# Kernel optimization log

Hardware: AMD Instinct MI355X
Metric: run time of the kernel (lower is better)

Reference implementation:

```python
import jax, jax.numpy as jnp
import numpy as np

G, K = 5, 3  # pyKAN defaults: grid intervals, spline order

def b_splines(x, grid, k=K):
    # x: [B, in], grid: [in, G+2k+1] extended knots -> basis [B, in, G+k]
    x = x[..., None]
    B = ((x >= grid[:, :-1]) & (x < grid[:, 1:])).astype(x.dtype)
    for p in range(1, k + 1):  # De Boor / Cox recursion
        B = (x - grid[:, :-(p + 1)]) / (grid[:, p:-1] - grid[:, :-(p + 1)]) * B[..., :-1] \
          + (grid[:, p + 1:] - x) / (grid[:, p + 1:] - grid[:, 1:-p]) * B[..., 1:]
    return B

def kan_layer(x, grid, coef, scale_base, scale_sp):
    # y_j = sum_i scale_base[i,j]*silu(x_i) + scale_sp[i,j]*sum_k coef[i,j,k]*B_k(x_i)
    basis = b_splines(x, grid)                                  # [B, in, G+K]
    y_sp = jnp.einsum('bik,iok,io->bo', basis, coef, scale_sp)
    y_base = jnp.einsum('bi,io->bo', jax.nn.silu(x), scale_base)
    return y_base + y_sp

def _uniform_grid(dim, g=G, k=K):
    h = 2.0 / g
    knots = np.linspace(-1.0 - k * h, 1.0 + k * h, g + 2 * k + 1).astype(np.float32)
    return jnp.tile(jnp.asarray(knots)[None, :], (dim, 1))

def setup_inputs() -> dict:
    key = jax.random.key(0)
    ks = jax.random.split(key, 7)
    B, IN, HID, OUT = 2048, 128, 512, 128
    nb = G + K
    return {
        'state': jax.random.normal(ks[0], (B, IN), jnp.float32),
        'grid1': _uniform_grid(IN),
        'coef1': 0.1 * jax.random.normal(ks[1], (IN, HID, nb), jnp.float32),
        'scale_base1': jax.random.normal(ks[2], (IN, HID), jnp.float32) / np.sqrt(IN).astype(np.float32),
        'scale_sp1': jnp.ones((IN, HID), jnp.float32),
        'grid2': _uniform_grid(HID),
        'coef2': 0.1 * jax.random.normal(ks[3], (HID, OUT, nb), jnp.float32),
        'scale_base2': jax.random.normal(ks[4], (HID, OUT), jnp.float32) / np.sqrt(HID).astype(np.float32),
        'scale_sp2': jnp.ones((HID, OUT), jnp.float32),
    }

def reference(state, grid1, coef1, scale_base1, scale_sp1, grid2, coef2, scale_base2, scale_sp2):
    h = kan_layer(state, grid1, coef1, scale_base1, scale_sp1)
    y = kan_layer(h, grid2, coef2, scale_base2, scale_sp2)
    return y
```

## Files before the change

kernel.cpp:

```cpp
#include <hip/hip_runtime.h>
#include <math.h>

#define BATCH 2048
#define IN1   128
#define HID   512
#define OUT2  128
#define NB    8
#define NKNOT 12
#define K1 (IN1*9)
#define K2 (HID*9)
#define SPLIT2 16
#define KS2 288
#define LDSW 40
#define A2S 296

typedef short s16x8 __attribute__((ext_vector_type(8)));
typedef float f32x4 __attribute__((ext_vector_type(4)));

__device__ inline unsigned short f2bf(float f) {
    unsigned int u = __float_as_uint(f);
    return (unsigned short)((u + 0x7fffu + ((u >> 16) & 1u)) >> 16);
}

__device__ inline void basis8(float x, float* out8) {
    float d[NKNOT];
#pragma unroll
    for (int t = 0; t < NKNOT; ++t) d[t] = x - (0.4f * (float)t - 2.2f);
    float B[NKNOT - 1];
#pragma unroll
    for (int t = 0; t < NKNOT - 1; ++t)
        B[t] = (d[t] >= 0.0f && d[t + 1] < 0.0f) ? 1.0f : 0.0f;
#pragma unroll
    for (int p = 1; p <= 3; ++p) {
        const float c = 1.0f / (0.4f * (float)p);
#pragma unroll
        for (int t = 0; t < NKNOT - 1; ++t)
            if (t < NKNOT - 1 - p)
                B[t] = c * (d[t] * B[t] - d[t + p + 1] * B[t + 1]);
    }
#pragma unroll
    for (int t = 0; t < NB; ++t) out8[t] = B[t];
}

__device__ inline float silu_f(float x) {
    return x * __builtin_amdgcn_rcpf(1.0f + __expf(-x));
}

__global__ __launch_bounds__(256) void prep(
        const float* __restrict__ state,
        const float* __restrict__ coef1, const float* __restrict__ sb1, const float* __restrict__ sp1,
        const float* __restrict__ coef2, const float* __restrict__ sb2, const float* __restrict__ sp2,
        unsigned short* __restrict__ Wt1, unsigned short* __restrict__ Wt2p,
        unsigned short* __restrict__ A1, float* __restrict__ outz) {
    const int gt = blockIdx.x * 256 + threadIdx.x;
    const int NT = gridDim.x * 256;

    for (int idx = gt; idx < (BATCH * OUT2) / 4; idx += NT)
        ((f32x4*)outz)[idx] = (f32x4){0.f, 0.f, 0.f, 0.f};

    for (int i = gt; i < IN1 * HID; i += NT) {
        int ii = i / HID, o = i % HID;
        float sp = sp1[(size_t)ii * HID + o];
        const float* c = coef1 + ((size_t)ii * HID + o) * NB;
        s16x8 v;
#pragma unroll
        for (int k = 0; k < 8; ++k) v[k] = (short)f2bf(c[k] * sp);
        *(s16x8*)(Wt1 + (size_t)o * K1 + ii * 8) = v;
    }
    for (int t = gt; t < HID * IN1; t += NT) {
        int o = t / IN1, i = t % IN1;
        Wt1[(size_t)o * K1 + IN1 * 8 + i] = f2bf(sb1[(size_t)i * HID + o]);
    }
    for (int i = gt; i < HID * OUT2; i += NT) {
        int ii = i / OUT2, o = i % OUT2;
        int z = ii >> 5, il = ii & 31;
        float sp = sp2[(size_t)ii * OUT2 + o];
        const float* c = coef2 + ((size_t)ii * OUT2 + o) * NB;
        s16x8 v;
#pragma unroll
        for (int k = 0; k < 8; ++k) v[k] = (short)f2bf(c[k] * sp);
        *(s16x8*)(Wt2p + (size_t)o * K2 + z * KS2 + il * 8) = v;
    }
    for (int t = gt; t < OUT2 * HID; t += NT) {
        int o = t / HID, i = t % HID;
        int z = i >> 5, il = i & 31;
        Wt2p[(size_t)o * K2 + z * KS2 + 256 + il] = f2bf(sb2[(size_t)i * OUT2 + o]);
    }
    for (int idx = gt; idx < BATCH * IN1; idx += NT) {
        int b = idx >> 7, i = idx & 127;
        float x = state[idx];
        float Bv[NB];
        basis8(x, Bv);
        s16x8 v;
#pragma unroll
        for (int t = 0; t < NB; ++t) v[t] = (short)f2bf(Bv[t]);
        *(s16x8*)(A1 + (size_t)b * K1 + i * 8) = v;
        A1[(size_t)b * K1 + IN1 * 8 + i] = f2bf(silu_f(x));
    }
}

__global__ __launch_bounds__(256) void gemm1(const unsigned short* __restrict__ A,
                                             const unsigned short* __restrict__ Wt1,
                                             float* __restrict__ h) {
    __shared__ unsigned short As[2 * 32 * LDSW];
    __shared__ unsigned short Bs[2 * 64 * LDSW];
    constexpr int NIT = K1 / 32;
    const int col0 = blockIdx.x * 64;
    const int row0 = blockIdx.y * 32;
    const int tid  = threadIdx.x;
    const int wave = tid >> 6, lane = tid & 63;
    const int q  = lane >> 4, mn = lane & 15;
    const int wr = wave >> 1, wc = wave & 1;
    const int srow = tid >> 2, chunk = (tid & 3) * 8;
    const bool doA = (wave < 2);
    const int srowA = srow & 31;

    const unsigned short* Ag = A   + (size_t)(row0 + srowA) * K1 + chunk;
    const unsigned short* Bg = Wt1 + (size_t)(col0 + srow)  * K1 + chunk;
    const int swA = srowA * LDSW + chunk;
    const int swB = srow  * LDSW + chunk;

    f32x4 acc0 = {0,0,0,0}, acc1 = {0,0,0,0};
    s16x8 gaN = {0,0,0,0,0,0,0,0}, gaN2 = gaN, gbN, gbN2;
    {
        s16x8 g0b = *(const s16x8*)Bg;
        *(s16x8*)&Bs[swB] = g0b;
        if (doA) { s16x8 g0a = *(const s16x8*)Ag; *(s16x8*)&As[swA] = g0a; }
    }
    gbN  = *(const s16x8*)(Bg + 32);
    gbN2 = *(const s16x8*)(Bg + 64);
    if (doA) { gaN = *(const s16x8*)(Ag + 32); gaN2 = *(const s16x8*)(Ag + 64); }

#pragma unroll 2
    for (int it = 0; it < NIT; ++it) {
        __syncthreads();
        if (it + 1 < NIT) {
            *(s16x8*)&Bs[((it + 1) & 1) * (64 * LDSW) + swB] = gbN;
            if (doA) *(s16x8*)&As[((it + 1) & 1) * (32 * LDSW) + swA] = gaN;
            gbN = gbN2;
            if (doA) gaN = gaN2;
            if (it + 3 < NIT) {
                gbN2 = *(const s16x8*)(Bg + (it + 3) * 32);
                if (doA) gaN2 = *(const s16x8*)(Ag + (it + 3) * 32);
            }
        }
        const unsigned short* Ab = &As[(it & 1) * (32 * LDSW)];
        const unsigned short* Bb = &Bs[(it & 1) * (64 * LDSW)];
        s16x8 af = *(const s16x8*)&Ab[(wr * 16 + mn) * LDSW + q * 8];
        s16x8 b0 = *(const s16x8*)&Bb[(wc * 32      + mn) * LDSW + q * 8];
        s16x8 b1 = *(const s16x8*)&Bb[(wc * 32 + 16 + mn) * LDSW + q * 8];
        acc0 = __builtin_amdgcn_mfma_f32_16x16x32_bf16(af, b0, acc0, 0, 0, 0);
        acc1 = __builtin_amdgcn_mfma_f32_16x16x32_bf16(af, b1, acc1, 0, 0, 0);
    }

    f32x4 accs[2] = {acc0, acc1};
#pragma unroll
    for (int ci = 0; ci < 2; ++ci)
#pragma unroll
        for (int r = 0; r < 4; ++r) {
            int gr = row0 + wr * 16 + q * 4 + r;
            int gc = col0 + wc * 32 + ci * 16 + mn;
            h[(size_t)gr * HID + gc] = accs[ci][r];
        }
}

__global__ __launch_bounds__(256) void gemm2(const float* __restrict__ h,
                                             const unsigned short* __restrict__ Wt,
                                             float* __restrict__ out) {
    __shared__ unsigned short a2[64 * A2S];
    __shared__ unsigned short Bs[2 * 128 * LDSW];
    constexpr int NIT = KS2 / 32;
    const int row0 = blockIdx.x * 64;
    const int z    = blockIdx.y;
    const int k0   = z * KS2;
    const int tid  = threadIdx.x;
    const int wave = tid >> 6, lane = tid & 63;
    const int q  = lane >> 4, mn = lane & 15;
    const int wrh = wave & 1;
    const int wch = wave >> 1;

    {
        int r  = tid >> 2;
        int c0 = (tid & 3) * 8;
        const float* hp = h + (size_t)(row0 + r) * HID + z * 32 + c0;
        f32x4 h0 = *(const f32x4*)hp;
        f32x4 h1 = *(const f32x4*)(hp + 4);
#pragma unroll
        for (int j = 0; j < 8; ++j) {
            float x = (j < 4) ? h0[j] : h1[j - 4];
            float Bv[NB];
            basis8(x, Bv);
            s16x8 v;
#pragma unroll
            for (int t = 0; t < NB; ++t) v[t] = (short)f2bf(Bv[t]);
            *(s16x8*)&a2[r * A2S + (c0 + j) * 8] = v;
            a2[r * A2S + 256 + c0 + j] = f2bf(silu_f(x));
        }
    }

    const int browB0 = tid >> 2,         chunkB = (tid & 3) * 8;
    const int browB1 = (tid + 256) >> 2;
    const unsigned short* BgB0 = Wt + (size_t)browB0 * K2 + k0 + chunkB;
    const unsigned short* BgB1 = Wt + (size_t)browB1 * K2 + k0 + chunkB;
    const int swB0 = browB0 * LDSW + chunkB;
    const int swB1 = browB1 * LDSW + chunkB;

    f32x4 acc[2][4];
#pragma unroll
    for (int a = 0; a < 2; ++a)
#pragma unroll
        for (int b = 0; b < 4; ++b) acc[a][b] = (f32x4){0.f, 0.f, 0.f, 0.f};

    {
        s16x8 g0b0 = *(const s16x8*)BgB0;
        s16x8 g0b1 = *(const s16x8*)BgB1;
        *(s16x8*)&Bs[swB0] = g0b0;
        *(s16x8*)&Bs[swB1] = g0b1;
    }
    s16x8 gb0N  = *(const s16x8*)(BgB0 + 32);
    s16x8 gb1N  = *(const s16x8*)(BgB1 + 32);
    s16x8 gb0N2 = *(const s16x8*)(BgB0 + 64);
    s16x8 gb1N2 = *(const s16x8*)(BgB1 + 64);

#pragma unroll
    for (int it = 0; it < NIT; ++it) {
        __syncthreads();
        if (it + 1 < NIT) {
            *(s16x8*)&Bs[((it + 1) & 1) * (128 * LDSW) + swB0] = gb0N;
            *(s16x8*)&Bs[((it + 1) & 1) * (128 * LDSW) + swB1] = gb1N;
            gb0N = gb0N2; gb1N = gb1N2;
            if (it + 3 < NIT) {
                gb0N2 = *(const s16x8*)(BgB0 + (it + 3) * 32);
                gb1N2 = *(const s16x8*)(BgB1 + (it + 3) * 32);
            }
        }
        const unsigned short* Bb = &Bs[(it & 1) * (128 * LDSW)];
        s16x8 af0 = *(const s16x8*)&a2[(wrh * 32      + mn) * A2S + it * 32 + q * 8];
        s16x8 af1 = *(const s16x8*)&a2[(wrh * 32 + 16 + mn) * A2S + it * 32 + q * 8];
        s16x8 bf[4];
#pragma unroll
        for (int nt = 0; nt < 4; ++nt)
            bf[nt] = *(const s16x8*)&Bb[(wch * 64 + nt * 16 + mn) * LDSW + q * 8];
#pragma unroll
        for (int nt = 0; nt < 4; ++nt) {
            acc[0][nt] = __builtin_amdgcn_mfma_f32_16x16x32_bf16(af0, bf[nt], acc[0][nt], 0, 0, 0);
            acc[1][nt] = __builtin_amdgcn_mfma_f32_16x16x32_bf16(af1, bf[nt], acc[1][nt], 0, 0, 0);
        }
    }

#pragma unroll
    for (int rf = 0; rf < 2; ++rf)
#pragma unroll
        for (int nt = 0; nt < 4; ++nt)
#pragma unroll
            for (int r = 0; r < 4; ++r) {
                int grow = row0 + wrh * 32 + rf * 16 + q * 4 + r;
                int gcol = wch * 64 + nt * 16 + mn;
                unsafeAtomicAdd(&out[(size_t)grow * OUT2 + gcol], acc[rf][nt][r]);
            }
}

extern "C" void kernel_launch(void* const* d_in, const int* in_sizes, int n_in,
                              void* d_out, int out_size, void* d_ws, size_t ws_size,
                              hipStream_t stream) {
    const float* state = (const float*)d_in[0];
    const float* coef1 = (const float*)d_in[2];
    const float* sb1   = (const float*)d_in[3];
    const float* sp1   = (const float*)d_in[4];
    const float* coef2 = (const float*)d_in[6];
    const float* sb2   = (const float*)d_in[7];
    const float* sp2   = (const float*)d_in[8];
    float* out = (float*)d_out;

    char* ws = (char*)d_ws;
    size_t off = 0;
    unsigned short* Wt1  = (unsigned short*)(ws + off); off += (size_t)K1 * HID  * 2;
    unsigned short* Wt2p = (unsigned short*)(ws + off); off += (size_t)K2 * OUT2 * 2;
    unsigned short* A1   = (unsigned short*)(ws + off); off += (size_t)BATCH * K1 * 2;
    float* h             = (float*)(ws + off);          off += (size_t)BATCH * HID * 4;
    (void)ws_size;

    prep<<<512, 256, 0, stream>>>(state, coef1, sb1, sp1, coef2, sb2, sp2, Wt1, Wt2p, A1, out);

    gemm1<<<dim3(8, 64), 256, 0, stream>>>(A1, Wt1, h);

    gemm2<<<dim3(32, SPLIT2), 256, 0, stream>>>(h, Wt2p, out);
}
```

Baseline: 115.9 us.

## Replace split-K atomic accumulation with partial buffers and in-kernel counter reduction

gemm2 now writes each split-K slice's partial tile to its own workspace buffer instead of atomically adding into the output. A per-row-block counter acts as a grid barrier across the 16 split blocks, and each block then sums all 16 partials for a 4-row slice and writes the final output. This also removes zeroing the output in prep. The cost is 16 MB of extra partial-buffer traffic plus a spin-wait. The spin-wait relies on all 16 blocks of a row group being co-resident (512 blocks total), otherwise it could deadlock.

```diff
diff --git a/kernel.cpp b/kernel.cpp
--- a/kernel.cpp
+++ b/kernel.cpp
@@ -16,6 +16,7 @@
 
 typedef short s16x8 __attribute__((ext_vector_type(8)));
 typedef float f32x4 __attribute__((ext_vector_type(4)));
+typedef float f32x2 __attribute__((ext_vector_type(2)));
 
 __device__ inline unsigned short f2bf(float f) {
     unsigned int u = __float_as_uint(f);
@@ -51,12 +52,11 @@
         const float* __restrict__ coef1, const float* __restrict__ sb1, const float* __restrict__ sp1,
         const float* __restrict__ coef2, const float* __restrict__ sb2, const float* __restrict__ sp2,
         unsigned short* __restrict__ Wt1, unsigned short* __restrict__ Wt2p,
-        unsigned short* __restrict__ A1, float* __restrict__ outz) {
+        unsigned short* __restrict__ A1, unsigned int* __restrict__ cnt) {
     const int gt = blockIdx.x * 256 + threadIdx.x;
     const int NT = gridDim.x * 256;
 
-    for (int idx = gt; idx < (BATCH * OUT2) / 4; idx += NT)
-        ((f32x4*)outz)[idx] = (f32x4){0.f, 0.f, 0.f, 0.f};
+    if (gt < 32) cnt[gt] = 0u;
 
     for (int i = gt; i < IN1 * HID; i += NT) {
         int ii = i / HID, o = i % HID;
@@ -166,6 +166,8 @@
 
 __global__ __launch_bounds__(256) void gemm2(const float* __restrict__ h,
                                              const unsigned short* __restrict__ Wt,
+                                             float* __restrict__ Cpart,
+                                             unsigned int* __restrict__ cnt,
                                              float* __restrict__ out) {
     __shared__ unsigned short a2[64 * A2S];
     __shared__ unsigned short Bs[2 * 128 * LDSW];
@@ -248,6 +250,7 @@
         }
     }
 
+    float* C = Cpart + (size_t)z * BATCH * OUT2;
 #pragma unroll
     for (int rf = 0; rf < 2; ++rf)
 #pragma unroll
@@ -256,8 +259,32 @@
             for (int r = 0; r < 4; ++r) {
                 int grow = row0 + wrh * 32 + rf * 16 + q * 4 + r;
                 int gcol = wch * 64 + nt * 16 + mn;
-                unsafeAtomicAdd(&out[(size_t)grow * OUT2 + gcol], acc[rf][nt][r]);
+                C[(size_t)grow * OUT2 + gcol] = acc[rf][nt][r];
             }
+
+    __threadfence();
+    __syncthreads();
+    if (tid == 0) {
+        atomicAdd(&cnt[blockIdx.x], 1u);
+        while (__hip_atomic_load(&cnt[blockIdx.x], __ATOMIC_ACQUIRE,
+                                 __HIP_MEMORY_SCOPE_AGENT) < (unsigned)SPLIT2)
+            __builtin_amdgcn_s_sleep(1);
+    }
+    __syncthreads();
+
+    {
+        int e  = tid * 2;
+        int rr = e >> 7;
+        int cc = e & 127;
+        size_t base = (size_t)(row0 + z * 4 + rr) * OUT2 + cc;
+        f32x2 s = {0.f, 0.f};
+#pragma unroll
+        for (int zz = 0; zz < SPLIT2; ++zz) {
+            f32x2 p = *(const f32x2*)(Cpart + (size_t)zz * BATCH * OUT2 + base);
+            s += p;
+        }
+        *(f32x2*)(out + base) = s;
+    }
 }
 
 extern "C" void kernel_launch(void* const* d_in, const int* in_sizes, int n_in,
@@ -278,11 +305,13 @@
     unsigned short* Wt2p = (unsigned short*)(ws + off); off += (size_t)K2 * OUT2 * 2;
     unsigned short* A1   = (unsigned short*)(ws + off); off += (size_t)BATCH * K1 * 2;
     float* h             = (float*)(ws + off);          off += (size_t)BATCH * HID * 4;
+    float* op            = (float*)(ws + off);          off += (size_t)SPLIT2 * BATCH * OUT2 * 4;
+    unsigned int* cnt    = (unsigned int*)(ws + off);   off += 32 * sizeof(unsigned int);
     (void)ws_size;
 
-    prep<<<512, 256, 0, stream>>>(state, coef1, sb1, sp1, coef2, sb2, sp2, Wt1, Wt2p, A1, out);
+    prep<<<512, 256, 0, stream>>>(state, coef1, sb1, sp1, coef2, sb2, sp2, Wt1, Wt2p, A1, cnt);
 
     gemm1<<<dim3(8, 64), 256, 0, stream>>>(A1, Wt1, h);
 
-    gemm2<<<dim3(32, SPLIT2), 256, 0, stream>>>(h, Wt2p, out);
-}
+    gemm2<<<dim3(32, SPLIT2), 256, 0, stream>>>(h, Wt2p, op, cnt, out);
+}
```

Result: slower. 206.3 us (+78.0%).
